# Optimization experiments

Measured on AMD Instinct MI355X. Metric: run time of the kernel, lower is better.

## Reference

```python
import math
import jax, jax.numpy as jnp
import numpy as np

AZI = 0.006135923151542565
INC = 0.008267349088394194
EPS = 1e-6
NUM_GROUPS = 32


def group_norm(x, weight, bias, num_groups=NUM_GROUPS, eps=EPS):
    B, C, H, W = x.shape
    xg = x.reshape(B, num_groups, C // num_groups, H, W)
    mean = xg.mean(axis=(2, 3, 4), keepdims=True)
    var = xg.var(axis=(2, 3, 4), keepdims=True)
    xg = (xg - mean) * jax.lax.rsqrt(var + eps)
    x = xg.reshape(B, C, H, W)
    return x * weight[None, :, None, None] + bias[None, :, None, None]


def conv1x1(x, w, b):
    # x: [B,C,H,W], w: [O,C], b: [O]
    return jnp.einsum('bchw,oc->bohw', x, w) + b[None, :, None, None]


def edge_conv(x, r, w1, b1, w2, b2, azi=AZI, inc=INC):
    out = None
    for shift_h in (-1, 0, 1):
        for shift_w in (-1, 0, 1):
            x_s = jnp.roll(x, shift=(shift_w, shift_h), axis=(2, 3))
            r_s = jnp.roll(r, shift=(shift_w, shift_h), axis=(2, 3))
            ca, sa = math.cos(shift_w * azi), math.sin(shift_w * azi)
            ci, si = math.cos(shift_h * inc), math.sin(shift_h * inc)
            pe0 = r_s * (ca * ci) - r
            pe1 = r_s * (ca * si)
            pe2 = r_s * sa
            inp = jnp.concatenate((x_s, x, pe0, pe1, pe2), axis=1)
            h = jax.nn.relu(conv1x1(inp, w1, b1))
            h = conv1x1(h, w2, b2)
            out = h if out is None else jnp.maximum(out, h)
    return out


def setup_inputs() -> dict:
    key = jax.random.key(0)
    ks = jax.random.split(key, 12)
    B, C, W, H = 4, 64, 64, 1024
    O = 64
    Cin1 = 2 * C + 3
    Cin2 = 2 * O + 3

    def lin(k, o, i):
        return jax.random.normal(k, (o, i), dtype=jnp.float32) * (1.0 / np.sqrt(i))

    return {
        'x': jax.random.normal(ks[0], (B, C, W, H), dtype=jnp.float32),
        'r': jax.random.uniform(ks[1], (B, 1, W, H), dtype=jnp.float32),
        'n1_w': jnp.ones((C,), jnp.float32),
        'n1_b': jnp.zeros((C,), jnp.float32),
        'c1_w1': lin(ks[2], O, Cin1),
        'c1_b1': jnp.zeros((O,), jnp.float32),
        'c1_w2': lin(ks[3], O, O),
        'c1_b2': jnp.zeros((O,), jnp.float32),
        'n2_w': jnp.ones((O,), jnp.float32),
        'n2_b': jnp.zeros((O,), jnp.float32),
        'c2_w1': lin(ks[4], O, Cin2),
        'c2_b1': jnp.zeros((O,), jnp.float32),
        'c2_w2': lin(ks[5], O, O),
        'c2_b2': jnp.zeros((O,), jnp.float32),
    }


def reference(x, r, n1_w, n1_b, c1_w1, c1_b1, c1_w2, c1_b2,
              n2_w, n2_b, c2_w1, c2_b1, c2_w2, c2_b2):
    h = group_norm(x, n1_w, n1_b)
    h = jax.nn.relu(h)
    h = edge_conv(h, r, c1_w1, c1_b1, c1_w2, c1_b2)
    h = group_norm(h, n2_w, n2_b)
    h = jax.nn.relu(h)
    # dropout p=0.0 -> identity
    h = edge_conv(h, r, c2_w1, c2_b1, c2_w2, c2_b2)
    return x + h
```

## Files before the change

### kernel.cpp

```cpp
#include <hip/hip_runtime.h>
#include <hip/hip_bf16.h>
#include <cmath>
#include <math.h>

namespace {

constexpr int Bn = 4;
constexpr int Cn = 64;
constexpr int Wn = 64;
constexpr int Hn = 1024;
constexpr int HWn = Wn * Hn;
constexpr int CHWn = Cn * HWn;

typedef float f32x4 __attribute__((ext_vector_type(4)));
typedef short bf16x8 __attribute__((ext_vector_type(8)));
union Frag { uint4 u; bf16x8 s; };

constexpr float kCA[3] = {0.9999811753f, 1.0f, 0.9999811753f};
constexpr float kSA[3] = {-0.0061358846f, 0.0f, 0.0061358846f};
constexpr float kCI[3] = {0.9999658257f, 1.0f, 0.9999658257f};
constexpr float kSI[3] = {-0.0082672549f, 0.0f, 0.0082672549f};

__device__ inline unsigned packbf(float a, float b) {
  union { __hip_bfloat162 h; unsigned u; } c;
  c.h = __float22bfloat162_rn(make_float2(a, b));
  return c.u;
}
__device__ inline float bflo(unsigned d) { return __uint_as_float(d << 16); }
__device__ inline float bfhi(unsigned d) { return __uint_as_float(d & 0xFFFF0000u); }

__device__ inline void gload16(const void* g, void* l) {
  __builtin_amdgcn_global_load_lds(
      (const __attribute__((address_space(1))) void*)g,
      (__attribute__((address_space(3))) void*)l, 16, 0, 0);
}

__global__ __launch_bounds__(256) void gn_partial_kernel(
    const float* __restrict__ x, float* __restrict__ partial) {
  const int bg = blockIdx.x >> 4, part = blockIdx.x & 15;
  const float4* base = (const float4*)(x + (size_t)bg * 2 * HWn) + part * 2048;
  float s = 0.f, s2 = 0.f;
  for (int i = threadIdx.x; i < 2048; i += 256) {
    const float4 v = base[i];
    s += v.x + v.y + v.z + v.w;
    s2 += v.x * v.x + v.y * v.y + v.z * v.z + v.w * v.w;
  }
  #pragma unroll
  for (int off = 32; off > 0; off >>= 1) {
    s  += __shfl_down(s, off, 64);
    s2 += __shfl_down(s2, off, 64);
  }
  __shared__ float red[8];
  const int wid = threadIdx.x >> 6, lid = threadIdx.x & 63;
  if (lid == 0) { red[wid * 2] = s; red[wid * 2 + 1] = s2; }
  __syncthreads();
  if (threadIdx.x == 0) {
    float ts = red[0] + red[2] + red[4] + red[6];
    float t2 = red[1] + red[3] + red[5] + red[7];
    atomicAdd(&partial[bg * 2], ts);
    atomicAdd(&partial[bg * 2 + 1], t2);
  }
}

__global__ void gn_final_kernel(const float* __restrict__ partial,
                                float* __restrict__ stats) {
  const int i = threadIdx.x;
  if (i < 128) {
    const float inv = 1.0f / (2.0f * HWn);
    const float mean = partial[2 * i] * inv;
    const float var = partial[2 * i + 1] * inv - mean * mean;
    stats[2 * i] = mean;
    stats[2 * i + 1] = rsqrtf(var + 1e-6f);
  }
}

__global__ void pack_weights_kernel(const float* __restrict__ w1,
                                    const float* __restrict__ w2,
                                    ushort* __restrict__ w1a, ushort* __restrict__ w1b,
                                    ushort* __restrict__ w2p,
                                    float* __restrict__ vs9, float* __restrict__ pw0) {
  const int t = threadIdx.x;
  for (int i = t; i < 64 * 32; i += 256) {
    const int o = i >> 5, kp = (i & 31) * 2;
    *(unsigned*)&w1a[o * 64 + kp] = packbf(w1[o * 131 + kp], w1[o * 131 + kp + 1]);
    *(unsigned*)&w1b[o * 64 + kp] = packbf(w1[o * 131 + 64 + kp], w1[o * 131 + 64 + kp + 1]);
    *(unsigned*)&w2p[o * 64 + kp] = packbf(w2[o * 64 + kp], w2[o * 64 + kp + 1]);
  }
  if (t < 64) pw0[t] = w1[t * 131 + 128];
  for (int i = t; i < 9 * 64; i += 256) {
    const int s = i >> 6, k = i & 63;
    const int isw = s / 3, ish = s % 3;
    const float m0 = kCA[isw] * kCI[ish];
    const float m1 = kCA[isw] * kSI[ish];
    const float m2 = kSA[isw];
    vs9[s * 64 + k] = m0 * w1[k * 131 + 128] + m1 * w1[k * 131 + 129] +
                      m2 * w1[k * 131 + 130];
  }
}

__global__ __launch_bounds__(256, 3) void dual_gemm_kernel(
    const float* __restrict__ x, const float* __restrict__ stats,
    const float* __restrict__ gw, const float* __restrict__ gb,
    const ushort* __restrict__ w1a, const ushort* __restrict__ w1b,
    const float* __restrict__ b1,
    ushort* __restrict__ Y, ushort* __restrict__ Z) {
  __shared__ float2 scsh[64];
  __shared__ float bias[64];
  __shared__ __align__(16) ushort dsY[64 * 72];
  __shared__ __align__(16) ushort dsZ[64 * 72];
  const int blk = blockIdx.x;
  const int h0 = (blk & 15) * 64;
  const int w  = (blk >> 4) & 63;
  const int b  = blk >> 10;
  const int t  = threadIdx.x;
  const int lane = t & 63, wv = t >> 6;
  const int n = lane & 15, q = lane >> 4;

  if (t < 64) {
    const int g = t >> 1;
    const float mean = stats[(b * 32 + g) * 2];
    const float rstd = stats[(b * 32 + g) * 2 + 1];
    const float sc = rstd * gw[t];
    scsh[t] = make_float2(sc, gb[t] - mean * sc);
    bias[t] = b1[t];
  }
  __syncthreads();

  const int jg = h0 + wv * 16 + n;
  const float* xb = x + (size_t)b * CHWn + (size_t)w * Hn;
  Frag Bf[2];
  #pragma unroll
  for (int kh = 0; kh < 2; kh++) {
    unsigned d[4];
    #pragma unroll
    for (int p = 0; p < 4; p++) {
      const int c0 = kh * 32 + q * 8 + p * 2;
      const float2 s0 = scsh[c0], s1 = scsh[c0 + 1];
      const float v0 = fmaxf(xb[(size_t)c0 * HWn + jg] * s0.x + s0.y, 0.f);
      const float v1 = fmaxf(xb[(size_t)(c0 + 1) * HWn + jg] * s1.x + s1.y, 0.f);
      d[p] = packbf(v0, v1);
    }
    Bf[kh].u = make_uint4(d[0], d[1], d[2], d[3]);
  }

  f32x4 accY[4], accZ[4];
  #pragma unroll
  for (int os = 0; os < 4; os++) { accY[os] = (f32x4)0.f; accZ[os] = (f32x4)0.f; }

  #pragma unroll
  for (int os = 0; os < 4; os++) {
    const int o = os * 16 + n;
    #pragma unroll
    for (int kh = 0; kh < 2; kh++) {
      const int k = kh * 32 + q * 8;
      Frag fa, fb;
      fa.u = *(const uint4*)&w1a[o * 64 + k];
      fb.u = *(const uint4*)&w1b[o * 64 + k];
      accY[os] = __builtin_amdgcn_mfma_f32_16x16x32_bf16(fa.s, Bf[kh].s, accY[os], 0, 0, 0);
      accZ[os] = __builtin_amdgcn_mfma_f32_16x16x32_bf16(fb.s, Bf[kh].s, accZ[os], 0, 0, 0);
    }
  }

  const int jl = wv * 16 + n;
  #pragma unroll
  for (int os = 0; os < 4; os++) {
    #pragma unroll
    for (int rp = 0; rp < 4; rp += 2) {
      const int o = os * 16 + q * 4 + rp;
      *(unsigned*)&dsY[jl * 72 + o] = packbf(accY[os][rp], accY[os][rp + 1]);
      *(unsigned*)&dsZ[jl * 72 + o] =
          packbf(accZ[os][rp] + bias[o], accZ[os][rp + 1] + bias[o + 1]);
    }
  }
  __syncthreads();

  #pragma unroll
  for (int p = 0; p < 2; p++) {
    const int slot = t + 256 * p;
    const int j = slot >> 3, og = slot & 7;
    const size_t gidx = (((size_t)b * Wn + w) * Hn + h0 + j) * 64 + og * 8;
    *(uint4*)&Y[gidx] = *(const uint4*)&dsY[j * 72 + og * 8];
    *(uint4*)&Z[gidx] = *(const uint4*)&dsZ[j * 72 + og * 8];
  }
}

__global__ __launch_bounds__(256, 3) void shift_max_kernel(
    const ushort* __restrict__ Y, const ushort* __restrict__ Z,
    const float* __restrict__ r, const float* __restrict__ vs9,
    const float* __restrict__ pw0, const ushort* __restrict__ w2p,
    const float* __restrict__ b2,
    const float* __restrict__ xres, const int add_res,
    float* __restrict__ out) {
  __shared__ __align__(16) ushort ys[2][66 * 64];
  __shared__ __align__(16) ushort w2l[64 * 64];
  __shared__ float rsh[3][68];
  __shared__ __align__(16) float vsl[9 * 64];
  const int blk = blockIdx.x;
  const int h0 = (blk & 15) * 64;
  const int w  = (blk >> 4) & 63;
  const int b  = blk >> 10;
  const int t  = threadIdx.x;
  const int lane = t & 63, wv = t >> 6;
  const int n = lane & 15, q = lane >> 4;
  const int jl = wv * 16 + n;

  const ushort* Yb = Y + (size_t)b * (size_t)Wn * Hn * 64;

  auto stage_col = [&](int bufidx, int wsrc) {
    const size_t ybase = (size_t)wsrc * (Hn * 64);
    #pragma unroll
    for (int p = 0; p < 3; p++) {
      const int slot = t + 256 * p;
      if (slot < 66 * 8) {
        const int jj = slot >> 3, S = slot & 7;
        const int G = S ^ (jj & 7);
        const int hsrc = (h0 + jj - 1 + 1024) & 1023;
        gload16(&Yb[ybase + (size_t)hsrc * 64 + G * 8],
                &ys[bufidx][(wv * 64 + 256 * p) * 8]);
      }
    }
  };

  stage_col(0, (w + 1) & 63);

  #pragma unroll
  for (int i0 = 0; i0 < 2; i0++) {
    const int i = t + i0 * 256;
    const int o = i >> 3, g = i & 7;
    *(uint4*)&w2l[o * 64 + (g ^ (o & 7)) * 8] = *(const uint4*)&w2p[o * 64 + g * 8];
  }
  if (t < 144) ((float4*)vsl)[t] = ((const float4*)vs9)[t];
  for (int i = t; i < 3 * 66; i += 256) {
    const int wi = i / 66, jj = i - wi * 66;
    const int wsrc = (w + wi - 1 + 64) & 63;
    const int hsrc = (h0 + jj - 1 + 1024) & 1023;
    rsh[wi][jj] = r[(size_t)b * HWn + wsrc * Hn + hsrc];
  }

  const float rc = r[(size_t)b * HWn + (size_t)w * Hn + h0 + jl];
  float zcA[8], zcB[8];
  {
    const size_t zbase = (((size_t)b * Wn + w) * Hn + h0 + jl) * 64;
    const uint4 z0 = *(const uint4*)&Z[zbase + q * 8];
    const uint4 z1 = *(const uint4*)&Z[zbase + 32 + q * 8];
    const float4 pwA0 = *(const float4*)&pw0[q * 8];
    const float4 pwA1 = *(const float4*)&pw0[q * 8 + 4];
    const float4 pwB0 = *(const float4*)&pw0[32 + q * 8];
    const float4 pwB1 = *(const float4*)&pw0[32 + q * 8 + 4];
    const float pwA[8] = {pwA0.x, pwA0.y, pwA0.z, pwA0.w, pwA1.x, pwA1.y, pwA1.z, pwA1.w};
    const float pwB[8] = {pwB0.x, pwB0.y, pwB0.z, pwB0.w, pwB1.x, pwB1.y, pwB1.z, pwB1.w};
    const unsigned zw0[4] = {z0.x, z0.y, z0.z, z0.w};
    const unsigned zw1[4] = {z1.x, z1.y, z1.z, z1.w};
    #pragma unroll
    for (int p = 0; p < 4; p++) {
      zcA[2 * p]     = bflo(zw0[p]) - rc * pwA[2 * p];
      zcA[2 * p + 1] = bfhi(zw0[p]) - rc * pwA[2 * p + 1];
      zcB[2 * p]     = bflo(zw1[p]) - rc * pwB[2 * p];
      zcB[2 * p + 1] = bfhi(zw1[p]) - rc * pwB[2 * p + 1];
    }
  }

  __syncthreads();

  f32x4 om[4];
  #pragma unroll
  for (int os = 0; os < 4; os++) om[os] = (f32x4)(-INFINITY);

  int cur = 0;
  for (int sw = -1; sw <= 1; sw++) {
    const int isw = sw + 1;
    if (sw < 1) stage_col(cur ^ 1, (w - (sw + 1) + 64) & 63);

    #pragma unroll
    for (int sh = -1; sh <= 1; sh++) {
      const int ish = sh + 1;
      const float rsv = rsh[1 - sw][jl - sh + 1];
      const float* vrow = &vsl[(isw * 3 + ish) * 64];
      const int ro = jl - sh + 1;
      Frag Bf0, Bf1;
      {
        const float4 vA0 = *(const float4*)&vrow[q * 8];
        const float4 vA1 = *(const float4*)&vrow[q * 8 + 4];
        const float vsA[8] = {vA0.x, vA0.y, vA0.z, vA0.w, vA1.x, vA1.y, vA1.z, vA1.w};
        const uint4 y0 = *(const uint4*)&ys[cur][ro * 64 + (q ^ (ro & 7)) * 8];
        const unsigned yw0[4] = {y0.x, y0.y, y0.z, y0.w};
        unsigned hw0[4];
        #pragma unroll
        for (int p = 0; p < 4; p++) {
          const float hA0 = fmaf(rsv, vsA[2 * p],     bflo(yw0[p]) + zcA[2 * p]);
          const float hA1 = fmaf(rsv, vsA[2 * p + 1], bfhi(yw0[p]) + zcA[2 * p + 1]);
          hw0[p] = packbf(fmaxf(hA0, 0.f), fmaxf(hA1, 0.f));
        }
        Bf0.u = make_uint4(hw0[0], hw0[1], hw0[2], hw0[3]);
      }
      {
        const float4 vB0 = *(const float4*)&vrow[32 + q * 8];
        const float4 vB1 = *(const float4*)&vrow[32 + q * 8 + 4];
        const float vsB[8] = {vB0.x, vB0.y, vB0.z, vB0.w, vB1.x, vB1.y, vB1.z, vB1.w};
        const uint4 y1 = *(const uint4*)&ys[cur][ro * 64 + ((q + 4) ^ (ro & 7)) * 8];
        const unsigned yw1[4] = {y1.x, y1.y, y1.z, y1.w};
        unsigned hw1[4];
        #pragma unroll
        for (int p = 0; p < 4; p++) {
          const float hB0 = fmaf(rsv, vsB[2 * p],     bflo(yw1[p]) + zcB[2 * p]);
          const float hB1 = fmaf(rsv, vsB[2 * p + 1], bfhi(yw1[p]) + zcB[2 * p + 1]);
          hw1[p] = packbf(fmaxf(hB0, 0.f), fmaxf(hB1, 0.f));
        }
        Bf1.u = make_uint4(hw1[0], hw1[1], hw1[2], hw1[3]);
      }
      #pragma unroll
      for (int os = 0; os < 4; os++) {
        const int orow = (os * 16 + n) * 64;
        Frag fa0, fa1;
        fa0.u = *(const uint4*)&w2l[orow + (q ^ (n & 7)) * 8];
        fa1.u = *(const uint4*)&w2l[orow + ((4 + q) ^ (n & 7)) * 8];
        f32x4 acc = (f32x4)0.f;
        acc = __builtin_amdgcn_mfma_f32_16x16x32_bf16(fa0.s, Bf0.s, acc, 0, 0, 0);
        acc = __builtin_amdgcn_mfma_f32_16x16x32_bf16(fa1.s, Bf1.s, acc, 0, 0, 0);
        #pragma unroll
        for (int e = 0; e < 4; e++) om[os][e] = fmaxf(om[os][e], acc[e]);
      }
    }

    if (sw < 1) {
      __syncthreads();
      cur ^= 1;
    }
  }

  const int jgl = h0 + jl;
  #pragma unroll
  for (int os = 0; os < 4; os++) {
    #pragma unroll
    for (int e = 0; e < 4; e++) {
      const int o = os * 16 + q * 4 + e;
      const size_t idx = ((size_t)b * Cn + o) * HWn + (size_t)w * Hn + jgl;
      float v = om[os][e] + b2[o];
      if (add_res) v += xres[idx];
      out[idx] = v;
    }
  }
}

}

extern "C" void kernel_launch(void* const* d_in, const int* in_sizes, int n_in,
                              void* d_out, int out_size, void* d_ws, size_t ws_size,
                              hipStream_t stream) {
  const float* x    = (const float*)d_in[0];
  const float* r    = (const float*)d_in[1];
  const float* n1w  = (const float*)d_in[2];
  const float* n1b  = (const float*)d_in[3];
  const float* c1w1 = (const float*)d_in[4];
  const float* c1b1 = (const float*)d_in[5];
  const float* c1w2 = (const float*)d_in[6];
  const float* c1b2 = (const float*)d_in[7];
  const float* n2w  = (const float*)d_in[8];
  const float* n2b  = (const float*)d_in[9];
  const float* c2w1 = (const float*)d_in[10];
  const float* c2b1 = (const float*)d_in[11];
  const float* c2w2 = (const float*)d_in[12];
  const float* c2b2 = (const float*)d_in[13];
  float* out = (float*)d_out;

  float* partial = (float*)d_ws;
  float* statsf  = partial + 256;
  float* vs9     = partial + 512;
  float* pw0     = partial + 1088;
  ushort* Ybf = (ushort*)((char*)d_ws + 8192);
  ushort* Zbf = Ybf + (size_t)Bn * Wn * Hn * 64;
  ushort* w1a = Zbf + (size_t)Bn * Wn * Hn * 64;
  ushort* w1b = w1a + 64 * 64;
  ushort* w2p = w1b + 64 * 64;

  hipMemsetAsync(partial, 0, 256 * sizeof(float), stream);
  gn_partial_kernel<<<2048, 256, 0, stream>>>(x, partial);
  gn_final_kernel<<<1, 128, 0, stream>>>(partial, statsf);
  pack_weights_kernel<<<1, 256, 0, stream>>>(c1w1, c1w2, w1a, w1b, w2p, vs9, pw0);
  dual_gemm_kernel<<<4096, 256, 0, stream>>>(x, statsf, n1w, n1b, w1a, w1b, c1b1, Ybf, Zbf);
  shift_max_kernel<<<4096, 256, 0, stream>>>(Ybf, Zbf, r, vs9, pw0, w2p, c1b2, x, 0, out);
  hipMemsetAsync(partial, 0, 256 * sizeof(float), stream);
  gn_partial_kernel<<<2048, 256, 0, stream>>>(out, partial);
  gn_final_kernel<<<1, 128, 0, stream>>>(partial, statsf);
  pack_weights_kernel<<<1, 256, 0, stream>>>(c2w1, c2w2, w1a, w1b, w2p, vs9, pw0);
  dual_gemm_kernel<<<4096, 256, 0, stream>>>(out, statsf, n2w, n2b, w1a, w1b, c2b1, Ybf, Zbf);
  shift_max_kernel<<<4096, 256, 0, stream>>>(Ybf, Zbf, r, vs9, pw0, w2p, c2b2, x, 1, out);
}
```

Baseline: 375.6 us.

## Stage x tile via LDS in dual GEMM; preload all three Y columns upfront

In the dual GEMM kernel, the x tile is now loaded into a swizzled LDS buffer with 16-byte async global loads, replacing strided scalar global reads per lane. In the shift-max kernel, the double-buffered per-column Y staging is replaced by loading all three neighbouring columns up front, which removes the in-loop syncthreads and lets the sw loop fully unroll. This costs extra LDS (about 16KB more in each kernel), which may lower occupancy below the launch-bounds target, and all column loads now finish before any compute starts instead of overlapping with it.

```diff
diff --git a/kernel.cpp b/kernel.cpp
--- a/kernel.cpp
+++ b/kernel.cpp
@@ -106,6 +106,7 @@
     ushort* __restrict__ Y, ushort* __restrict__ Z) {
   __shared__ float2 scsh[64];
   __shared__ float bias[64];
+  __shared__ __align__(16) float xl[64 * 16 * 4];
   __shared__ __align__(16) ushort dsY[64 * 72];
   __shared__ __align__(16) ushort dsZ[64 * 72];
   const int blk = blockIdx.x;
@@ -116,6 +117,15 @@
   const int lane = t & 63, wv = t >> 6;
   const int n = lane & 15, q = lane >> 4;
 
+  const float* xb = x + (size_t)b * CHWn + (size_t)w * Hn;
+  #pragma unroll
+  for (int p = 0; p < 4; p++) {
+    const int slot = t + 256 * p;
+    const int c = slot >> 4, g = slot & 15;
+    const int G = g ^ (c & 15);
+    gload16(&xb[(size_t)c * HWn + h0 + G * 4], &xl[(wv * 64 + 256 * p) * 4]);
+  }
+
   if (t < 64) {
     const int g = t >> 1;
     const float mean = stats[(b * 32 + g) * 2];
@@ -126,8 +136,8 @@
   }
   __syncthreads();
 
-  const int jg = h0 + wv * 16 + n;
-  const float* xb = x + (size_t)b * CHWn + (size_t)w * Hn;
+  const int jloc = wv * 16 + n;
+  const int g0 = jloc >> 2, w0 = jloc & 3;
   Frag Bf[2];
   #pragma unroll
   for (int kh = 0; kh < 2; kh++) {
@@ -136,8 +146,10 @@
     for (int p = 0; p < 4; p++) {
       const int c0 = kh * 32 + q * 8 + p * 2;
       const float2 s0 = scsh[c0], s1 = scsh[c0 + 1];
-      const float v0 = fmaxf(xb[(size_t)c0 * HWn + jg] * s0.x + s0.y, 0.f);
-      const float v1 = fmaxf(xb[(size_t)(c0 + 1) * HWn + jg] * s1.x + s1.y, 0.f);
+      const float xv0 = xl[(c0 * 16 + (g0 ^ (c0 & 15))) * 4 + w0];
+      const float xv1 = xl[((c0 + 1) * 16 + (g0 ^ ((c0 + 1) & 15))) * 4 + w0];
+      const float v0 = fmaxf(xv0 * s0.x + s0.y, 0.f);
+      const float v1 = fmaxf(xv1 * s1.x + s1.y, 0.f);
       d[p] = packbf(v0, v1);
     }
     Bf[kh].u = make_uint4(d[0], d[1], d[2], d[3]);
@@ -191,7 +203,7 @@
     const float* __restrict__ b2,
     const float* __restrict__ xres, const int add_res,
     float* __restrict__ out) {
-  __shared__ __align__(16) ushort ys[2][66 * 64];
+  __shared__ __align__(16) ushort ys3[3][66 * 64];
   __shared__ __align__(16) ushort w2l[64 * 64];
   __shared__ float rsh[3][68];
   __shared__ __align__(16) float vsl[9 * 64];
@@ -206,7 +218,7 @@
 
   const ushort* Yb = Y + (size_t)b * (size_t)Wn * Hn * 64;
 
-  auto stage_col = [&](int bufidx, int wsrc) {
+  auto stage_col = [&](int wi, int wsrc) {
     const size_t ybase = (size_t)wsrc * (Hn * 64);
     #pragma unroll
     for (int p = 0; p < 3; p++) {
@@ -216,12 +228,14 @@
         const int G = S ^ (jj & 7);
         const int hsrc = (h0 + jj - 1 + 1024) & 1023;
         gload16(&Yb[ybase + (size_t)hsrc * 64 + G * 8],
-                &ys[bufidx][(wv * 64 + 256 * p) * 8]);
+                &ys3[wi][(wv * 64 + 256 * p) * 8]);
       }
     }
   };
 
-  stage_col(0, (w + 1) & 63);
+  stage_col(0, (w + 63) & 63);
+  stage_col(1, w);
+  stage_col(2, (w + 1) & 63);
 
   #pragma unroll
   for (int i0 = 0; i0 < 2; i0++) {
@@ -266,11 +280,10 @@
   #pragma unroll
   for (int os = 0; os < 4; os++) om[os] = (f32x4)(-INFINITY);
 
-  int cur = 0;
+  #pragma unroll
   for (int sw = -1; sw <= 1; sw++) {
     const int isw = sw + 1;
-    if (sw < 1) stage_col(cur ^ 1, (w - (sw + 1) + 64) & 63);
-
+    const ushort* ysb = ys3[1 - sw];
     #pragma unroll
     for (int sh = -1; sh <= 1; sh++) {
       const int ish = sh + 1;
@@ -282,7 +295,7 @@
         const float4 vA0 = *(const float4*)&vrow[q * 8];
         const float4 vA1 = *(const float4*)&vrow[q * 8 + 4];
         const float vsA[8] = {vA0.x, vA0.y, vA0.z, vA0.w, vA1.x, vA1.y, vA1.z, vA1.w};
-        const uint4 y0 = *(const uint4*)&ys[cur][ro * 64 + (q ^ (ro & 7)) * 8];
+        const uint4 y0 = *(const uint4*)&ysb[ro * 64 + (q ^ (ro & 7)) * 8];
         const unsigned yw0[4] = {y0.x, y0.y, y0.z, y0.w};
         unsigned hw0[4];
         #pragma unroll
@@ -297,7 +310,7 @@
         const float4 vB0 = *(const float4*)&vrow[32 + q * 8];
         const float4 vB1 = *(const float4*)&vrow[32 + q * 8 + 4];
         const float vsB[8] = {vB0.x, vB0.y, vB0.z, vB0.w, vB1.x, vB1.y, vB1.z, vB1.w};
-        const uint4 y1 = *(const uint4*)&ys[cur][ro * 64 + ((q + 4) ^ (ro & 7)) * 8];
+        const uint4 y1 = *(const uint4*)&ysb[ro * 64 + ((q + 4) ^ (ro & 7)) * 8];
         const unsigned yw1[4] = {y1.x, y1.y, y1.z, y1.w};
         unsigned hw1[4];
         #pragma unroll
@@ -321,11 +334,6 @@
         for (int e = 0; e < 4; e++) om[os][e] = fmaxf(om[os][e], acc[e]);
       }
     }
-
-    if (sw < 1) {
-      __syncthreads();
-      cur ^= 1;
-    }
   }
 
   const int jgl = h0 + jl;
```

Result: slower. 432.5 us (+15.1%).
